# Kernel tuning notes

Measured on AMD Instinct MI355X. Metric: run time of the kernel, lower is better.

Reference implementation:

```python
import jax, jax.numpy as jnp
import numpy as np

B, S, D_MODEL, D_K = 4, 2048, 1024, 1
D_QKV = D_MODEL * D_K  # per-stream feature dim (q, k, v each)
MASK_NEG = -9000000000000000.0


def setup_inputs() -> dict:
    key = jax.random.key(0)
    kx, kw = jax.random.split(key)
    x = jax.random.normal(kx, (B, S, D_MODEL), dtype=jnp.float32)
    # Dense kernel, flax convention: [in_features, out_features], no bias
    W = jax.random.normal(kw, (D_MODEL, 3 * D_QKV), dtype=jnp.float32) * (1.0 / np.sqrt(D_MODEL))
    return {"x": x, "W": W}


def _scaled_dot_product_attention(q, k, v):
    # q,k,v: [B, S, d]
    d_k = k.shape[-1]
    scores = jnp.einsum("bqd,bkd->bqk", q, k) / jnp.sqrt(jnp.float32(d_k))
    # Faithful to source: keep upper triangle (incl. diagonal), then mask zeros.
    scores = jnp.triu(scores, k=0)
    scores = jnp.where(scores == 0, MASK_NEG, scores)
    attn = jax.nn.softmax(scores, axis=-1)
    return jnp.einsum("bqk,bkd->bqd", attn, v)


def reference(x, W) -> jnp.ndarray:
    qkv = jnp.einsum("bsd,df->bsf", x, W)  # fused QKV projection
    q, k, v = jnp.split(qkv, 3, axis=-1)
    return _scaled_dot_product_attention(q, k, v)
```

## Files before the change

### kernel.cpp

```cpp
#include <hip/hip_runtime.h>

#define SB 2048
#define DM 1024
#define N3 3072

typedef short bf16x8 __attribute__((ext_vector_type(8)));
typedef float f32x4 __attribute__((ext_vector_type(4)));
typedef unsigned short u16;

#define MFMA16(a, b, c) __builtin_amdgcn_mfma_f32_16x16x32_bf16(a, b, c, 0, 0, 0)

typedef const __attribute__((address_space(1))) unsigned int* gptr_t;
typedef __attribute__((address_space(3))) unsigned int* lptr_t;

__device__ __forceinline__ u16 f2bf(float x) {
  union { float f; unsigned u; } c; c.f = x;
  unsigned r = c.u + 0x7FFFu + ((c.u >> 16) & 1u);
  return (u16)(r >> 16);
}
__device__ __forceinline__ float bf2f(u16 x) {
  union { unsigned u; float f; } c; c.u = ((unsigned)x) << 16;
  return c.f;
}

__global__ void k_cvt_x(const float* __restrict__ x, u16* __restrict__ xb, int n4) {
  int i = blockIdx.x * blockDim.x + threadIdx.x;
  if (i >= n4) return;
  float4 v = ((const float4*)x)[i];
  ushort4 o;
  o.x = f2bf(v.x); o.y = f2bf(v.y); o.z = f2bf(v.z); o.w = f2bf(v.w);
  ((ushort4*)xb)[i] = o;
}

__global__ void k_cvt_wt(const float* __restrict__ W, u16* __restrict__ Wt) {
  __shared__ float t[32][33];
  int n0 = blockIdx.x * 32;
  int k0 = blockIdx.y * 32;
  int tx = threadIdx.x & 31, ty = threadIdx.x >> 5;
#pragma unroll
  for (int r = 0; r < 4; ++r)
    t[ty + r * 8][tx] = W[(size_t)(k0 + ty + r * 8) * N3 + n0 + tx];
  __syncthreads();
#pragma unroll
  for (int r = 0; r < 4; ++r)
    Wt[(size_t)(n0 + ty + r * 8) * DM + k0 + tx] = f2bf(t[tx][ty + r * 8]);
}

__global__ __launch_bounds__(256, 2) void k_gemm(const u16* __restrict__ xb,
                                                 const u16* __restrict__ wt,
                                                 u16* __restrict__ qk,
                                                 u16* __restrict__ vt) {
  __shared__ u16 As[2][128 * 32];
  __shared__ u16 Bs[2][128 * 32];
  int mt = blockIdx.x / 24, nt = blockIdx.x % 24;
  int m0 = mt * 128, n0 = nt * 128;
  int tid = threadIdx.x, lane = tid & 63, wid = tid >> 6;
  int lr = lane & 15, lg = lane >> 4;
  int wm = (wid >> 1) * 64, wn = (wid & 1) * 64;
  int ca = lane >> 2;
  int cb = (lane & 3) * 8;
  f32x4 acc[4][4] = {};
  int p = 0;
  for (int kk = 0; kk < 1024; kk += 32) {
#pragma unroll
    for (int j = 0; j < 2; ++j) {
      int chunk = wid * 2 + j;
      const u16* ga = xb + (size_t)(m0 + chunk * 16 + ca) * 1024 + kk + cb;
      const u16* gb = wt + (size_t)(n0 + chunk * 16 + ca) * 1024 + kk + cb;
      __builtin_amdgcn_global_load_lds((gptr_t)(const void*)ga, (lptr_t)(void*)&As[p][chunk * 512], 16, 0, 0);
      __builtin_amdgcn_global_load_lds((gptr_t)(const void*)gb, (lptr_t)(void*)&Bs[p][chunk * 512], 16, 0, 0);
    }
    __syncthreads();
    bf16x8 af[4], bff[4];
#pragma unroll
    for (int i = 0; i < 4; ++i) af[i] = *(const bf16x8*)&As[p][(wm + i * 16 + lr) * 32 + lg * 8];
#pragma unroll
    for (int j = 0; j < 4; ++j) bff[j] = *(const bf16x8*)&Bs[p][(wn + j * 16 + lr) * 32 + lg * 8];
#pragma unroll
    for (int i = 0; i < 4; ++i)
#pragma unroll
      for (int j = 0; j < 4; ++j)
        acc[i][j] = MFMA16(af[i], bff[j], acc[i][j]);
    __syncthreads();
    p ^= 1;
  }
  if (nt < 16) {
#pragma unroll
    for (int i = 0; i < 4; ++i)
#pragma unroll
      for (int j = 0; j < 4; ++j)
#pragma unroll
        for (int r = 0; r < 4; ++r)
          qk[(size_t)(m0 + wm + i * 16 + lg * 4 + r) * 2048 + n0 + wn + j * 16 + lr] = f2bf(acc[i][j][r]);
  } else {
    int d0 = n0 - 2048;
#pragma unroll
    for (int i = 0; i < 4; ++i)
#pragma unroll
      for (int j = 0; j < 4; ++j)
#pragma unroll
        for (int r = 0; r < 4; ++r) {
          int m = m0 + wm + i * 16 + lg * 4 + r;
          int d = d0 + wn + j * 16 + lr;
          vt[(size_t)((m >> 11) * DM + d) * SB + (m & 2047)] = f2bf(acc[i][j][r]);
        }
  }
}

__global__ __launch_bounds__(256, 2) void k_qkt(const u16* __restrict__ qk,
                                                u16* __restrict__ S) {
  __shared__ u16 As[2][128 * 32];
  __shared__ u16 Bs[2][128 * 32];
  int bid = blockIdx.x;
  int b = bid & 3;
  int pi = bid >> 2;
  int qt = 0;
  while (true) { int cnt = 16 - qt; if (pi < cnt) break; pi -= cnt; ++qt; }
  int kt = qt + pi;
  int m0 = qt * 128, n0 = kt * 128;
  int tid = threadIdx.x, lane = tid & 63, wid = tid >> 6;
  int lr = lane & 15, lg = lane >> 4;
  int wm = (wid >> 1) * 64, wn = (wid & 1) * 64;
  int ca = lane >> 2;
  int cb = (lane & 3) * 8;
  const u16* Qb = qk + (size_t)(b * SB) * 2048;
  f32x4 acc[4][4] = {};
  int p = 0;
  for (int kk = 0; kk < 1024; kk += 32) {
#pragma unroll
    for (int j = 0; j < 2; ++j) {
      int chunk = wid * 2 + j;
      const u16* ga = Qb + (size_t)(m0 + chunk * 16 + ca) * 2048 + kk + cb;
      const u16* gb = Qb + (size_t)(n0 + chunk * 16 + ca) * 2048 + 1024 + kk + cb;
      __builtin_amdgcn_global_load_lds((gptr_t)(const void*)ga, (lptr_t)(void*)&As[p][chunk * 512], 16, 0, 0);
      __builtin_amdgcn_global_load_lds((gptr_t)(const void*)gb, (lptr_t)(void*)&Bs[p][chunk * 512], 16, 0, 0);
    }
    __syncthreads();
    bf16x8 af[4], bff[4];
#pragma unroll
    for (int i = 0; i < 4; ++i) af[i] = *(const bf16x8*)&As[p][(wm + i * 16 + lr) * 32 + lg * 8];
#pragma unroll
    for (int j = 0; j < 4; ++j) bff[j] = *(const bf16x8*)&Bs[p][(wn + j * 16 + lr) * 32 + lg * 8];
#pragma unroll
    for (int i = 0; i < 4; ++i)
#pragma unroll
      for (int j = 0; j < 4; ++j)
        acc[i][j] = MFMA16(af[i], bff[j], acc[i][j]);
    __syncthreads();
    p ^= 1;
  }
  u16* Sb = S + (size_t)(b * SB) * 2048;
#pragma unroll
  for (int i = 0; i < 4; ++i)
#pragma unroll
    for (int j = 0; j < 4; ++j)
#pragma unroll
      for (int r = 0; r < 4; ++r) {
        int q = m0 + wm + i * 16 + lg * 4 + r;
        int k = n0 + wn + j * 16 + lr;
        float v = acc[i][j][r] * 0.03125f;
        if (k < q) v = -1e30f;
        Sb[(size_t)q * 2048 + k] = f2bf(v);
      }
}

__global__ void k_sm(u16* __restrict__ S) {
  __shared__ float rmax[4], rsum[4];
  int row = blockIdx.x;
  int q = row & 2047;
  int k0 = (q >> 7) << 7;
  int len = 2048 - k0;
  int tid = threadIdx.x;
  u16* rp = S + (size_t)row * 2048 + k0;
  int nv = len >> 3;
  bool act = tid < nv;
  float v[8];
  float mx = -1e30f;
  if (act) {
    bf16x8 x = *(const bf16x8*)(rp + tid * 8);
#pragma unroll
    for (int j = 0; j < 8; ++j) { v[j] = bf2f((u16)x[j]); mx = fmaxf(mx, v[j]); }
  }
#pragma unroll
  for (int off = 32; off; off >>= 1) mx = fmaxf(mx, __shfl_xor(mx, off, 64));
  int wv = tid >> 6;
  if ((tid & 63) == 0) rmax[wv] = mx;
  __syncthreads();
  mx = fmaxf(fmaxf(rmax[0], rmax[1]), fmaxf(rmax[2], rmax[3]));
  float sum = 0.f;
  if (act) {
#pragma unroll
    for (int j = 0; j < 8; ++j) { v[j] = __expf(v[j] - mx); sum += v[j]; }
  }
#pragma unroll
  for (int off = 32; off; off >>= 1) sum += __shfl_xor(sum, off, 64);
  if ((tid & 63) == 0) rsum[wv] = sum;
  __syncthreads();
  float inv = 1.f / ((rsum[0] + rsum[1]) + (rsum[2] + rsum[3]));
  if (act) {
    bf16x8 o;
#pragma unroll
    for (int j = 0; j < 8; ++j) o[j] = (short)f2bf(v[j] * inv);
    *(bf16x8*)(rp + tid * 8) = o;
  }
}

__global__ __launch_bounds__(256, 2) void k_pv(const u16* __restrict__ P,
                                               const u16* __restrict__ vt,
                                               float* __restrict__ out) {
  __shared__ u16 As[2][128 * 32];
  __shared__ u16 Bs[2][128 * 32];
  int bid = blockIdx.x;
  int qt = bid >> 5;
  int rem = bid & 31;
  int dt = rem >> 2;
  int b = rem & 3;
  int m0 = qt * 128, n0 = dt * 128;
  int tid = threadIdx.x, lane = tid & 63, wid = tid >> 6;
  int lr = lane & 15, lg = lane >> 4;
  int wm = (wid >> 1) * 64, wn = (wid & 1) * 64;
  int ca = lane >> 2;
  int cb = (lane & 3) * 8;
  const u16* Pb = P + (size_t)(b * SB) * 2048;
  const u16* Vb = vt + (size_t)(b * DM) * 2048;
  f32x4 acc[4][4] = {};
  int p = 0;
  for (int kk = m0; kk < 2048; kk += 32) {
#pragma unroll
    for (int j = 0; j < 2; ++j) {
      int chunk = wid * 2 + j;
      const u16* ga = Pb + (size_t)(m0 + chunk * 16 + ca) * 2048 + kk + cb;
      const u16* gb = Vb + (size_t)(n0 + chunk * 16 + ca) * 2048 + kk + cb;
      __builtin_amdgcn_global_load_lds((gptr_t)(const void*)ga, (lptr_t)(void*)&As[p][chunk * 512], 16, 0, 0);
      __builtin_amdgcn_global_load_lds((gptr_t)(const void*)gb, (lptr_t)(void*)&Bs[p][chunk * 512], 16, 0, 0);
    }
    __syncthreads();
    bf16x8 af[4], bff[4];
#pragma unroll
    for (int i = 0; i < 4; ++i) af[i] = *(const bf16x8*)&As[p][(wm + i * 16 + lr) * 32 + lg * 8];
#pragma unroll
    for (int j = 0; j < 4; ++j) bff[j] = *(const bf16x8*)&Bs[p][(wn + j * 16 + lr) * 32 + lg * 8];
#pragma unroll
    for (int i = 0; i < 4; ++i)
#pragma unroll
      for (int j = 0; j < 4; ++j)
        acc[i][j] = MFMA16(af[i], bff[j], acc[i][j]);
    __syncthreads();
    p ^= 1;
  }
#pragma unroll
  for (int i = 0; i < 4; ++i)
#pragma unroll
    for (int j = 0; j < 4; ++j)
#pragma unroll
      for (int r = 0; r < 4; ++r)
        out[(size_t)(b * SB + m0 + wm + i * 16 + lg * 4 + r) * DM + n0 + wn + j * 16 + lr] = acc[i][j][r];
}

extern "C" void kernel_launch(void* const* d_in, const int* in_sizes, int n_in,
                              void* d_out, int out_size, void* d_ws, size_t ws_size,
                              hipStream_t stream) {
  const float* x = (const float*)d_in[0];
  const float* W = (const float*)d_in[1];
  float* out = (float*)d_out;
  char* ws = (char*)d_ws;
  u16* qk = (u16*)(ws);
  u16* vt = (u16*)(ws + 33554432);
  u16* xb = (u16*)(ws + 50331648);
  u16* wt = (u16*)(ws + 67108864);
  u16* S  = (u16*)(ws + 50331648);

  k_cvt_x<<<8192, 256, 0, stream>>>(x, xb, 2097152);
  dim3 gw(96, 32);
  k_cvt_wt<<<gw, 256, 0, stream>>>(W, wt);
  k_gemm<<<1536, 256, 0, stream>>>(xb, wt, qk, vt);
  k_qkt<<<544, 256, 0, stream>>>(qk, S);
  k_sm<<<8192, 256, 0, stream>>>(S);
  k_pv<<<512, 256, 0, stream>>>(S, vt, out);
}
```

Baseline: 167.6 us.

## Restructure QKV GEMM with 128x256 tiles, 4-stage LDS pipeline and swizzle

The projection GEMM now uses 512-thread blocks computing 128x256 tiles with a four-deep global-to-LDS prefetch ring. Manual vmcnt waits and a single barrier per k-step replace the previous double-buffered load/sync/compute loop. LDS rows are XOR-style rotated to avoid bank conflicts, block ids are swizzled for L2 locality, and MFMA runs at raised priority. This aims to hide global load latency and raise MFMA utilization, at the cost of more LDS per block, which may lower occupancy.

Result: slower. 179.7 us (+7.2%).

```diff
diff --git a/kernel.cpp b/kernel.cpp
--- a/kernel.cpp
+++ b/kernel.cpp
@@ -46,63 +46,94 @@
     Wt[(size_t)(n0 + ty + r * 8) * DM + k0 + tx] = f2bf(t[tx][ty + r * 8]);
 }
 
-__global__ __launch_bounds__(256, 2) void k_gemm(const u16* __restrict__ xb,
+__global__ __launch_bounds__(512, 2) void k_gemm(const u16* __restrict__ xb,
                                                  const u16* __restrict__ wt,
                                                  u16* __restrict__ qk,
                                                  u16* __restrict__ vt) {
-  __shared__ u16 As[2][128 * 32];
-  __shared__ u16 Bs[2][128 * 32];
-  int mt = blockIdx.x / 24, nt = blockIdx.x % 24;
-  int m0 = mt * 128, n0 = nt * 128;
+  __shared__ u16 Asl[4][128 * 32];
+  __shared__ u16 Bsl[4][256 * 32];
+  int bid = blockIdx.x;
+  int swz = (bid & 7) * 96 + (bid >> 3);
+  int mt = swz / 12, nt = swz % 12;
+  int m0 = mt * 128, n0 = nt * 256;
   int tid = threadIdx.x, lane = tid & 63, wid = tid >> 6;
-  int lr = lane & 15, lg = lane >> 4;
-  int wm = (wid >> 1) * 64, wn = (wid & 1) * 64;
-  int ca = lane >> 2;
-  int cb = (lane & 3) * 8;
+  int lr = lane & 15, kg = lane >> 4;
+  int wm = (wid >> 2) * 64, wn = (wid & 3) * 64;
+
+  int arow = tid >> 2, aseg = tid & 3;
+  const u16* aptr = xb + (size_t)(m0 + arow) * 1024 + ((aseg - (arow >> 1)) & 3) * 8;
+  int brow0 = tid >> 2, brow1 = 128 + (tid >> 2), bseg = tid & 3;
+  const u16* bptr0 = wt + (size_t)(n0 + brow0) * 1024 + ((bseg - (brow0 >> 1)) & 3) * 8;
+  const u16* bptr1 = wt + (size_t)(n0 + brow1) * 1024 + ((bseg - (brow1 >> 1)) & 3) * 8;
+
   f32x4 acc[4][4] = {};
-  int p = 0;
-  for (int kk = 0; kk < 1024; kk += 32) {
-#pragma unroll
-    for (int j = 0; j < 2; ++j) {
-      int chunk = wid * 2 + j;
-      const u16* ga = xb + (size_t)(m0 + chunk * 16 + ca) * 1024 + kk + cb;
-      const u16* gb = wt + (size_t)(n0 + chunk * 16 + ca) * 1024 + kk + cb;
-      __builtin_amdgcn_global_load_lds((gptr_t)(const void*)ga, (lptr_t)(void*)&As[p][chunk * 512], 16, 0, 0);
-      __builtin_amdgcn_global_load_lds((gptr_t)(const void*)gb, (lptr_t)(void*)&Bs[p][chunk * 512], 16, 0, 0);
-    }
-    __syncthreads();
-    bf16x8 af[4], bff[4];
-#pragma unroll
-    for (int i = 0; i < 4; ++i) af[i] = *(const bf16x8*)&As[p][(wm + i * 16 + lr) * 32 + lg * 8];
-#pragma unroll
-    for (int j = 0; j < 4; ++j) bff[j] = *(const bf16x8*)&Bs[p][(wn + j * 16 + lr) * 32 + lg * 8];
-#pragma unroll
-    for (int i = 0; i < 4; ++i)
-#pragma unroll
-      for (int j = 0; j < 4; ++j)
-        acc[i][j] = MFMA16(af[i], bff[j], acc[i][j]);
-    __syncthreads();
-    p ^= 1;
-  }
-  if (nt < 16) {
-#pragma unroll
-    for (int i = 0; i < 4; ++i)
+
+#define STAGE_A(kt) __builtin_amdgcn_global_load_lds( \
+    (gptr_t)(const void*)(aptr + (kt) * 32), (lptr_t)(void*)&Asl[(kt) & 3][tid * 8], 16, 0, 0)
+#define STAGE_B(kt) do { \
+    __builtin_amdgcn_global_load_lds((gptr_t)(const void*)(bptr0 + (kt) * 32), \
+        (lptr_t)(void*)&Bsl[(kt) & 3][tid * 8], 16, 0, 0); \
+    __builtin_amdgcn_global_load_lds((gptr_t)(const void*)(bptr1 + (kt) * 32), \
+        (lptr_t)(void*)&Bsl[(kt) & 3][4096 + tid * 8], 16, 0, 0); } while (0)
+
+  STAGE_A(0); STAGE_B(0);
+  STAGE_A(1); STAGE_B(1);
+  STAGE_A(2); STAGE_B(2);
+  asm volatile("s_waitcnt vmcnt(6)" ::: "memory");
+  __builtin_amdgcn_s_barrier();
+
+  for (int i = 0; i < 32; ++i) {
+    int buf = i & 3;
+    if (i <= 28) STAGE_A(i + 3);
+    bf16x8 bfr[4], afr[4];
+#pragma unroll
+    for (int j = 0; j < 4; ++j) {
+      int row = wn + j * 16 + lr;
+      int slot = (kg + (row >> 1)) & 3;
+      bfr[j] = *(const bf16x8*)&Bsl[buf][row * 32 + slot * 8];
+    }
+#pragma unroll
+    for (int q = 0; q < 4; ++q) {
+      int row = wm + q * 16 + lr;
+      int slot = (kg + (row >> 1)) & 3;
+      afr[q] = *(const bf16x8*)&Asl[buf][row * 32 + slot * 8];
+    }
+    if (i <= 28) STAGE_B(i + 3);
+    __builtin_amdgcn_s_setprio(1);
+#pragma unroll
+    for (int q = 0; q < 4; ++q)
+#pragma unroll
+      for (int j = 0; j < 4; ++j)
+        acc[q][j] = MFMA16(afr[q], bfr[j], acc[q][j]);
+    __builtin_amdgcn_s_setprio(0);
+    if (i < 31) {
+      if (i <= 28)      asm volatile("s_waitcnt vmcnt(6)" ::: "memory");
+      else if (i == 29) asm volatile("s_waitcnt vmcnt(3)" ::: "memory");
+      else              asm volatile("s_waitcnt vmcnt(0)" ::: "memory");
+      __builtin_amdgcn_s_barrier();
+    }
+  }
+#undef STAGE_A
+#undef STAGE_B
+
+  if (n0 < 2048) {
+#pragma unroll
+    for (int q = 0; q < 4; ++q)
 #pragma unroll
       for (int j = 0; j < 4; ++j)
 #pragma unroll
         for (int r = 0; r < 4; ++r)
-          qk[(size_t)(m0 + wm + i * 16 + lg * 4 + r) * 2048 + n0 + wn + j * 16 + lr] = f2bf(acc[i][j][r]);
+          qk[(size_t)(m0 + wm + q * 16 + kg * 4 + r) * 2048 + n0 + wn + j * 16 + lr] = f2bf(acc[q][j][r]);
   } else {
-    int d0 = n0 - 2048;
-#pragma unroll
-    for (int i = 0; i < 4; ++i)
+#pragma unroll
+    for (int q = 0; q < 4; ++q)
 #pragma unroll
       for (int j = 0; j < 4; ++j)
 #pragma unroll
         for (int r = 0; r < 4; ++r) {
-          int m = m0 + wm + i * 16 + lg * 4 + r;
-          int d = d0 + wn + j * 16 + lr;
-          vt[(size_t)((m >> 11) * DM + d) * SB + (m & 2047)] = f2bf(acc[i][j][r]);
+          int m = m0 + wm + q * 16 + kg * 4 + r;
+          int d = n0 + wn + j * 16 + lr - 2048;
+          vt[(size_t)((m >> 11) * DM + d) * SB + (m & 2047)] = f2bf(acc[q][j][r]);
         }
   }
 }
@@ -273,7 +304,7 @@
   k_cvt_x<<<8192, 256, 0, stream>>>(x, xb, 2097152);
   dim3 gw(96, 32);
   k_cvt_wt<<<gw, 256, 0, stream>>>(W, wt);
-  k_gemm<<<1536, 256, 0, stream>>>(xb, wt, qk, vt);
+  k_gemm<<<768, 512, 0, stream>>>(xb, wt, qk, vt);
   k_qkt<<<544, 256, 0, stream>>>(qk, S);
   k_sm<<<8192, 256, 0, stream>>>(S);
   k_pv<<<512, 256, 0, stream>>>(S, vt, out);
```

## Add 4-buffer prefetch pipeline with swizzled LDS layout to the three GEMM kernels

Applied to the files above, without the earlier changes.

Reworks the GEMM, QK^T and PV kernels to use four LDS stages, prefetching two K-tiles ahead with global_load_lds. The previous loop synchronized twice per iteration with no overlap; the new loop uses a single s_waitcnt vmcnt plus a barrier per step. It also XOR-style rotates 16-byte segments per row pair to cut LDS bank conflicts on fragment reads, and raises wave priority around the MFMA block. LDS per block doubles to 64KB, which may limit occupancy to two blocks per CU as the launch bounds request.

Result: slower. 186.5 us (+11.3%).

```diff
diff --git a/kernel.cpp b/kernel.cpp
--- a/kernel.cpp
+++ b/kernel.cpp
@@ -21,6 +21,9 @@
 __device__ __forceinline__ float bf2f(u16 x) {
   union { unsigned u; float f; } c; c.u = ((unsigned)x) << 16;
   return c.f;
+}
+__device__ __forceinline__ void glds(const u16* g, u16* l) {
+  __builtin_amdgcn_global_load_lds((gptr_t)(const void*)g, (lptr_t)(void*)l, 16, 0, 0);
 }
 
 __global__ void k_cvt_x(const float* __restrict__ x, u16* __restrict__ xb, int n4) {
@@ -46,62 +49,82 @@
     Wt[(size_t)(n0 + ty + r * 8) * DM + k0 + tx] = f2bf(t[tx][ty + r * 8]);
 }
 
+
 __global__ __launch_bounds__(256, 2) void k_gemm(const u16* __restrict__ xb,
                                                  const u16* __restrict__ wt,
                                                  u16* __restrict__ qk,
                                                  u16* __restrict__ vt) {
-  __shared__ u16 As[2][128 * 32];
-  __shared__ u16 Bs[2][128 * 32];
-  int mt = blockIdx.x / 24, nt = blockIdx.x % 24;
+  __shared__ u16 As[4][128 * 32];
+  __shared__ u16 Bs[4][128 * 32];
+  int bid = blockIdx.x;
+  int mt = bid / 24, nt = bid % 24;
   int m0 = mt * 128, n0 = nt * 128;
   int tid = threadIdx.x, lane = tid & 63, wid = tid >> 6;
-  int lr = lane & 15, lg = lane >> 4;
+  int lr = lane & 15, kg = lane >> 4;
   int wm = (wid >> 1) * 64, wn = (wid & 1) * 64;
-  int ca = lane >> 2;
-  int cb = (lane & 3) * 8;
+  int r2 = tid >> 2, seg = tid & 3;
+  int scol = ((seg - (r2 >> 1)) & 3) * 8;
+  const u16* a0 = xb + (size_t)(m0 + r2) * 1024 + scol;
+  const u16* a1 = xb + (size_t)(m0 + 64 + r2) * 1024 + scol;
+  const u16* b0 = wt + (size_t)(n0 + r2) * 1024 + scol;
+  const u16* b1 = wt + (size_t)(n0 + 64 + r2) * 1024 + scol;
+
+#define STAGE(kt) do { int _b = (kt) & 3; int _o = (kt) * 32;            \
+    glds(a0 + _o, &As[_b][tid * 8]);                                     \
+    glds(a1 + _o, &As[_b][2048 + tid * 8]);                              \
+    glds(b0 + _o, &Bs[_b][tid * 8]);                                     \
+    glds(b1 + _o, &Bs[_b][2048 + tid * 8]); } while (0)
+
   f32x4 acc[4][4] = {};
-  int p = 0;
-  for (int kk = 0; kk < 1024; kk += 32) {
-#pragma unroll
-    for (int j = 0; j < 2; ++j) {
-      int chunk = wid * 2 + j;
-      const u16* ga = xb + (size_t)(m0 + chunk * 16 + ca) * 1024 + kk + cb;
-      const u16* gb = wt + (size_t)(n0 + chunk * 16 + ca) * 1024 + kk + cb;
-      __builtin_amdgcn_global_load_lds((gptr_t)(const void*)ga, (lptr_t)(void*)&As[p][chunk * 512], 16, 0, 0);
-      __builtin_amdgcn_global_load_lds((gptr_t)(const void*)gb, (lptr_t)(void*)&Bs[p][chunk * 512], 16, 0, 0);
-    }
-    __syncthreads();
+  STAGE(0); STAGE(1);
+  asm volatile("s_waitcnt vmcnt(4)" ::: "memory");
+  __builtin_amdgcn_s_barrier();
+  for (int t = 0; t < 32; ++t) {
+    if (t < 30) STAGE(t + 2);
+    int buf = t & 3;
     bf16x8 af[4], bff[4];
 #pragma unroll
-    for (int i = 0; i < 4; ++i) af[i] = *(const bf16x8*)&As[p][(wm + i * 16 + lr) * 32 + lg * 8];
-#pragma unroll
-    for (int j = 0; j < 4; ++j) bff[j] = *(const bf16x8*)&Bs[p][(wn + j * 16 + lr) * 32 + lg * 8];
+    for (int i = 0; i < 4; ++i) {
+      int row = wm + i * 16 + lr;
+      af[i] = *(const bf16x8*)&As[buf][row * 32 + ((kg + (row >> 1)) & 3) * 8];
+    }
+#pragma unroll
+    for (int j = 0; j < 4; ++j) {
+      int row = wn + j * 16 + lr;
+      bff[j] = *(const bf16x8*)&Bs[buf][row * 32 + ((kg + (row >> 1)) & 3) * 8];
+    }
+    __builtin_amdgcn_s_setprio(1);
 #pragma unroll
     for (int i = 0; i < 4; ++i)
 #pragma unroll
       for (int j = 0; j < 4; ++j)
         acc[i][j] = MFMA16(af[i], bff[j], acc[i][j]);
-    __syncthreads();
-    p ^= 1;
-  }
-  if (nt < 16) {
+    __builtin_amdgcn_s_setprio(0);
+    if (t < 31) {
+      if (t < 30) asm volatile("s_waitcnt vmcnt(4)" ::: "memory");
+      else        asm volatile("s_waitcnt vmcnt(0)" ::: "memory");
+      __builtin_amdgcn_s_barrier();
+    }
+  }
+#undef STAGE
+
+  if (n0 < 2048) {
 #pragma unroll
     for (int i = 0; i < 4; ++i)
 #pragma unroll
       for (int j = 0; j < 4; ++j)
 #pragma unroll
         for (int r = 0; r < 4; ++r)
-          qk[(size_t)(m0 + wm + i * 16 + lg * 4 + r) * 2048 + n0 + wn + j * 16 + lr] = f2bf(acc[i][j][r]);
+          qk[(size_t)(m0 + wm + i * 16 + kg * 4 + r) * 2048 + n0 + wn + j * 16 + lr] = f2bf(acc[i][j][r]);
   } else {
-    int d0 = n0 - 2048;
 #pragma unroll
     for (int i = 0; i < 4; ++i)
 #pragma unroll
       for (int j = 0; j < 4; ++j)
 #pragma unroll
         for (int r = 0; r < 4; ++r) {
-          int m = m0 + wm + i * 16 + lg * 4 + r;
-          int d = d0 + wn + j * 16 + lr;
+          int m = m0 + wm + i * 16 + kg * 4 + r;
+          int d = n0 + wn + j * 16 + lr - 2048;
           vt[(size_t)((m >> 11) * DM + d) * SB + (m & 2047)] = f2bf(acc[i][j][r]);
         }
   }
@@ -109,8 +132,8 @@
 
 __global__ __launch_bounds__(256, 2) void k_qkt(const u16* __restrict__ qk,
                                                 u16* __restrict__ S) {
-  __shared__ u16 As[2][128 * 32];
-  __shared__ u16 Bs[2][128 * 32];
+  __shared__ u16 As[4][128 * 32];
+  __shared__ u16 Bs[4][128 * 32];
   int bid = blockIdx.x;
   int b = bid & 3;
   int pi = bid >> 2;
@@ -119,36 +142,55 @@
   int kt = qt + pi;
   int m0 = qt * 128, n0 = kt * 128;
   int tid = threadIdx.x, lane = tid & 63, wid = tid >> 6;
-  int lr = lane & 15, lg = lane >> 4;
+  int lr = lane & 15, kg = lane >> 4;
   int wm = (wid >> 1) * 64, wn = (wid & 1) * 64;
-  int ca = lane >> 2;
-  int cb = (lane & 3) * 8;
+  int r2 = tid >> 2, seg = tid & 3;
+  int scol = ((seg - (r2 >> 1)) & 3) * 8;
   const u16* Qb = qk + (size_t)(b * SB) * 2048;
+  const u16* a0 = Qb + (size_t)(m0 + r2) * 2048 + scol;
+  const u16* a1 = Qb + (size_t)(m0 + 64 + r2) * 2048 + scol;
+  const u16* b0 = Qb + (size_t)(n0 + r2) * 2048 + 1024 + scol;
+  const u16* b1 = Qb + (size_t)(n0 + 64 + r2) * 2048 + 1024 + scol;
+
+#define STAGE(kt_) do { int _b = (kt_) & 3; int _o = (kt_) * 32;         \
+    glds(a0 + _o, &As[_b][tid * 8]);                                     \
+    glds(a1 + _o, &As[_b][2048 + tid * 8]);                              \
+    glds(b0 + _o, &Bs[_b][tid * 8]);                                     \
+    glds(b1 + _o, &Bs[_b][2048 + tid * 8]); } while (0)
+
   f32x4 acc[4][4] = {};
-  int p = 0;
-  for (int kk = 0; kk < 1024; kk += 32) {
-#pragma unroll
-    for (int j = 0; j < 2; ++j) {
-      int chunk = wid * 2 + j;
-      const u16* ga = Qb + (size_t)(m0 + chunk * 16 + ca) * 2048 + kk + cb;
-      const u16* gb = Qb + (size_t)(n0 + chunk * 16 + ca) * 2048 + 1024 + kk + cb;
-      __builtin_amdgcn_global_load_lds((gptr_t)(const void*)ga, (lptr_t)(void*)&As[p][chunk * 512], 16, 0, 0);
-      __builtin_amdgcn_global_load_lds((gptr_t)(const void*)gb, (lptr_t)(void*)&Bs[p][chunk * 512], 16, 0, 0);
-    }
-    __syncthreads();
+  STAGE(0); STAGE(1);
+  asm volatile("s_waitcnt vmcnt(4)" ::: "memory");
+  __builtin_amdgcn_s_barrier();
+  for (int t = 0; t < 32; ++t) {
+    if (t < 30) STAGE(t + 2);
+    int buf = t & 3;
     bf16x8 af[4], bff[4];
 #pragma unroll
-    for (int i = 0; i < 4; ++i) af[i] = *(const bf16x8*)&As[p][(wm + i * 16 + lr) * 32 + lg * 8];
-#pragma unroll
-    for (int j = 0; j < 4; ++j) bff[j] = *(const bf16x8*)&Bs[p][(wn + j * 16 + lr) * 32 + lg * 8];
+    for (int i = 0; i < 4; ++i) {
+      int row = wm + i * 16 + lr;
+      af[i] = *(const bf16x8*)&As[buf][row * 32 + ((kg + (row >> 1)) & 3) * 8];
+    }
+#pragma unroll
+    for (int j = 0; j < 4; ++j) {
+      int row = wn + j * 16 + lr;
+      bff[j] = *(const bf16x8*)&Bs[buf][row * 32 + ((kg + (row >> 1)) & 3) * 8];
+    }
+    __builtin_amdgcn_s_setprio(1);
 #pragma unroll
     for (int i = 0; i < 4; ++i)
 #pragma unroll
       for (int j = 0; j < 4; ++j)
         acc[i][j] = MFMA16(af[i], bff[j], acc[i][j]);
-    __syncthreads();
-    p ^= 1;
-  }
+    __builtin_amdgcn_s_setprio(0);
+    if (t < 31) {
+      if (t < 30) asm volatile("s_waitcnt vmcnt(4)" ::: "memory");
+      else        asm volatile("s_waitcnt vmcnt(0)" ::: "memory");
+      __builtin_amdgcn_s_barrier();
+    }
+  }
+#undef STAGE
+
   u16* Sb = S + (size_t)(b * SB) * 2048;
 #pragma unroll
   for (int i = 0; i < 4; ++i)
@@ -156,7 +198,7 @@
     for (int j = 0; j < 4; ++j)
 #pragma unroll
       for (int r = 0; r < 4; ++r) {
-        int q = m0 + wm + i * 16 + lg * 4 + r;
+        int q = m0 + wm + i * 16 + kg * 4 + r;
         int k = n0 + wn + j * 16 + lr;
         float v = acc[i][j][r] * 0.03125f;
         if (k < q) v = -1e30f;
@@ -208,53 +250,73 @@
 __global__ __launch_bounds__(256, 2) void k_pv(const u16* __restrict__ P,
                                                const u16* __restrict__ vt,
                                                float* __restrict__ out) {
-  __shared__ u16 As[2][128 * 32];
-  __shared__ u16 Bs[2][128 * 32];
+  __shared__ u16 As[4][128 * 32];
+  __shared__ u16 Bs[4][128 * 32];
   int bid = blockIdx.x;
   int qt = bid >> 5;
   int rem = bid & 31;
   int dt = rem >> 2;
   int b = rem & 3;
   int m0 = qt * 128, n0 = dt * 128;
+  int nkt = (2048 - m0) >> 5;
   int tid = threadIdx.x, lane = tid & 63, wid = tid >> 6;
-  int lr = lane & 15, lg = lane >> 4;
+  int lr = lane & 15, kg = lane >> 4;
   int wm = (wid >> 1) * 64, wn = (wid & 1) * 64;
-  int ca = lane >> 2;
-  int cb = (lane & 3) * 8;
+  int r2 = tid >> 2, seg = tid & 3;
+  int scol = ((seg - (r2 >> 1)) & 3) * 8;
   const u16* Pb = P + (size_t)(b * SB) * 2048;
   const u16* Vb = vt + (size_t)(b * DM) * 2048;
+  const u16* a0 = Pb + (size_t)(m0 + r2) * 2048 + m0 + scol;
+  const u16* a1 = Pb + (size_t)(m0 + 64 + r2) * 2048 + m0 + scol;
+  const u16* b0 = Vb + (size_t)(n0 + r2) * 2048 + m0 + scol;
+  const u16* b1 = Vb + (size_t)(n0 + 64 + r2) * 2048 + m0 + scol;
+
+#define STAGE(kt_) do { int _b = (kt_) & 3; int _o = (kt_) * 32;         \
+    glds(a0 + _o, &As[_b][tid * 8]);                                     \
+    glds(a1 + _o, &As[_b][2048 + tid * 8]);                              \
+    glds(b0 + _o, &Bs[_b][tid * 8]);                                     \
+    glds(b1 + _o, &Bs[_b][2048 + tid * 8]); } while (0)
+
   f32x4 acc[4][4] = {};
-  int p = 0;
-  for (int kk = m0; kk < 2048; kk += 32) {
-#pragma unroll
-    for (int j = 0; j < 2; ++j) {
-      int chunk = wid * 2 + j;
-      const u16* ga = Pb + (size_t)(m0 + chunk * 16 + ca) * 2048 + kk + cb;
-      const u16* gb = Vb + (size_t)(n0 + chunk * 16 + ca) * 2048 + kk + cb;
-      __builtin_amdgcn_global_load_lds((gptr_t)(const void*)ga, (lptr_t)(void*)&As[p][chunk * 512], 16, 0, 0);
-      __builtin_amdgcn_global_load_lds((gptr_t)(const void*)gb, (lptr_t)(void*)&Bs[p][chunk * 512], 16, 0, 0);
-    }
-    __syncthreads();
+  STAGE(0); STAGE(1);
+  asm volatile("s_waitcnt vmcnt(4)" ::: "memory");
+  __builtin_amdgcn_s_barrier();
+  for (int t = 0; t < nkt; ++t) {
+    if (t + 2 < nkt) STAGE(t + 2);
+    int buf = t & 3;
     bf16x8 af[4], bff[4];
 #pragma unroll
-    for (int i = 0; i < 4; ++i) af[i] = *(const bf16x8*)&As[p][(wm + i * 16 + lr) * 32 + lg * 8];
-#pragma unroll
-    for (int j = 0; j < 4; ++j) bff[j] = *(const bf16x8*)&Bs[p][(wn + j * 16 + lr) * 32 + lg * 8];
+    for (int i = 0; i < 4; ++i) {
+      int row = wm + i * 16 + lr;
+      af[i] = *(const bf16x8*)&As[buf][row * 32 + ((kg + (row >> 1)) & 3) * 8];
+    }
+#pragma unroll
+    for (int j = 0; j < 4; ++j) {
+      int row = wn + j * 16 + lr;
+      bff[j] = *(const bf16x8*)&Bs[buf][row * 32 + ((kg + (row >> 1)) & 3) * 8];
+    }
+    __builtin_amdgcn_s_setprio(1);
 #pragma unroll
     for (int i = 0; i < 4; ++i)
 #pragma unroll
       for (int j = 0; j < 4; ++j)
         acc[i][j] = MFMA16(af[i], bff[j], acc[i][j]);
-    __syncthreads();
-    p ^= 1;
-  }
+    __builtin_amdgcn_s_setprio(0);
+    if (t + 1 < nkt) {
+      if (t + 2 < nkt) asm volatile("s_waitcnt vmcnt(4)" ::: "memory");
+      else             asm volatile("s_waitcnt vmcnt(0)" ::: "memory");
+      __builtin_amdgcn_s_barrier();
+    }
+  }
+#undef STAGE
+
 #pragma unroll
   for (int i = 0; i < 4; ++i)
 #pragma unroll
     for (int j = 0; j < 4; ++j)
 #pragma unroll
       for (int r = 0; r < 4; ++r)
-        out[(size_t)(b * SB + m0 + wm + i * 16 + lg * 4 + r) * DM + n0 + wn + j * 16 + lr] = acc[i][j][r];
+        out[(size_t)(b * SB + m0 + wm + i * 16 + kg * 4 + r) * DM + n0 + wn + j * 16 + lr] = acc[i][j][r];
 }
 
 extern "C" void kernel_launch(void* const* d_in, const int* in_sizes, int n_in,
```

## Rewrite QKV projection GEMM with 256x256 tiles and 4-stage async pipeline

Applied to the files above, without the earlier changes.

The QKV projection GEMM now uses 256x256 tiles with 512 threads and a 4-buffer LDS ring fed by global_load_lds, prefetching two k-steps ahead. Work is split into half-steps with explicit waitcnt and barriers, plus s_setprio around the MFMA bursts. LDS columns are XOR-swizzled to avoid bank conflicts, and the block index is remapped to improve L2 locality. The aim is to hide global-load latency and raise MFMA utilization, at the cost of fewer blocks (384), one block per CU and fragile hand-written wait counts.

Result: slower. 171.9 us (+2.6%).

```diff
diff --git a/kernel.cpp b/kernel.cpp
--- a/kernel.cpp
+++ b/kernel.cpp
@@ -21,6 +21,9 @@
 __device__ __forceinline__ float bf2f(u16 x) {
   union { unsigned u; float f; } c; c.u = ((unsigned)x) << 16;
   return c.f;
+}
+__device__ __forceinline__ void glds(const u16* g, u16* l) {
+  __builtin_amdgcn_global_load_lds((gptr_t)(const void*)g, (lptr_t)(void*)l, 16, 0, 0);
 }
 
 __global__ void k_cvt_x(const float* __restrict__ x, u16* __restrict__ xb, int n4) {
@@ -46,62 +49,104 @@
     Wt[(size_t)(n0 + ty + r * 8) * DM + k0 + tx] = f2bf(t[tx][ty + r * 8]);
 }
 
-__global__ __launch_bounds__(256, 2) void k_gemm(const u16* __restrict__ xb,
+__global__ __launch_bounds__(512, 1) void k_gemm(const u16* __restrict__ xb,
                                                  const u16* __restrict__ wt,
                                                  u16* __restrict__ qk,
                                                  u16* __restrict__ vt) {
-  __shared__ u16 As[2][128 * 32];
-  __shared__ u16 Bs[2][128 * 32];
-  int mt = blockIdx.x / 24, nt = blockIdx.x % 24;
-  int m0 = mt * 128, n0 = nt * 128;
+  __shared__ u16 As[4][256 * 32];
+  __shared__ u16 Bs[4][256 * 32];
+  int bid = blockIdx.x;
+  int swz = (bid & 7) * 48 + (bid >> 3);
+  int mt = swz / 12, nt = swz % 12;
+  int m0 = mt * 256, n0 = nt * 256;
   int tid = threadIdx.x, lane = tid & 63, wid = tid >> 6;
-  int lr = lane & 15, lg = lane >> 4;
-  int wm = (wid >> 1) * 64, wn = (wid & 1) * 64;
-  int ca = lane >> 2;
-  int cb = (lane & 3) * 8;
-  f32x4 acc[4][4] = {};
-  int p = 0;
-  for (int kk = 0; kk < 1024; kk += 32) {
-#pragma unroll
-    for (int j = 0; j < 2; ++j) {
-      int chunk = wid * 2 + j;
-      const u16* ga = xb + (size_t)(m0 + chunk * 16 + ca) * 1024 + kk + cb;
-      const u16* gb = wt + (size_t)(n0 + chunk * 16 + ca) * 1024 + kk + cb;
-      __builtin_amdgcn_global_load_lds((gptr_t)(const void*)ga, (lptr_t)(void*)&As[p][chunk * 512], 16, 0, 0);
-      __builtin_amdgcn_global_load_lds((gptr_t)(const void*)gb, (lptr_t)(void*)&Bs[p][chunk * 512], 16, 0, 0);
-    }
-    __syncthreads();
-    bf16x8 af[4], bff[4];
-#pragma unroll
-    for (int i = 0; i < 4; ++i) af[i] = *(const bf16x8*)&As[p][(wm + i * 16 + lr) * 32 + lg * 8];
-#pragma unroll
-    for (int j = 0; j < 4; ++j) bff[j] = *(const bf16x8*)&Bs[p][(wn + j * 16 + lr) * 32 + lg * 8];
+  int lr = lane & 15, kg = lane >> 4;
+  int wm = (wid >> 2) * 128, wn = (wid & 3) * 64;
+  int r2 = tid >> 2, seg = tid & 3;
+  int scol = ((seg - (r2 >> 1)) & 3) * 8;
+  const u16* a0 = xb + (size_t)(m0 + r2) * 1024 + scol;
+  const u16* a1 = xb + (size_t)(m0 + 128 + r2) * 1024 + scol;
+  const u16* b0 = wt + (size_t)(n0 + r2) * 1024 + scol;
+  const u16* b1 = wt + (size_t)(n0 + 128 + r2) * 1024 + scol;
+
+#define STAGE_A(kt) do { int _b = (kt) & 3; int _o = (kt) * 32;          \
+    glds(a0 + _o, &As[_b][tid * 8]);                                     \
+    glds(a1 + _o, &As[_b][4096 + tid * 8]); } while (0)
+#define STAGE_B(kt) do { int _b = (kt) & 3; int _o = (kt) * 32;          \
+    glds(b0 + _o, &Bs[_b][tid * 8]);                                     \
+    glds(b1 + _o, &Bs[_b][4096 + tid * 8]); } while (0)
+
+  f32x4 acc[8][4] = {};
+  STAGE_A(0); STAGE_B(0);
+  STAGE_A(1); STAGE_B(1);
+  asm volatile("s_waitcnt vmcnt(4)" ::: "memory");
+  __builtin_amdgcn_s_barrier();
+
+  for (int t = 0; t < 32; ++t) {
+    int buf = t & 3;
+    bf16x8 bff[4], af[4];
+#pragma unroll
+    for (int j = 0; j < 4; ++j) {
+      int row = wn + j * 16 + lr;
+      bff[j] = *(const bf16x8*)&Bs[buf][row * 32 + ((kg + (row >> 1)) & 3) * 8];
+    }
+#pragma unroll
+    for (int i = 0; i < 4; ++i) {
+      int row = wm + i * 16 + lr;
+      af[i] = *(const bf16x8*)&As[buf][row * 32 + ((kg + (row >> 1)) & 3) * 8];
+    }
+    if (t <= 29) STAGE_A(t + 2);
+    __builtin_amdgcn_s_barrier();
+    asm volatile("s_waitcnt lgkmcnt(0)" ::: "memory");
+    __builtin_amdgcn_sched_barrier(0);
+    __builtin_amdgcn_s_setprio(1);
 #pragma unroll
     for (int i = 0; i < 4; ++i)
 #pragma unroll
       for (int j = 0; j < 4; ++j)
         acc[i][j] = MFMA16(af[i], bff[j], acc[i][j]);
-    __syncthreads();
-    p ^= 1;
-  }
-  if (nt < 16) {
+    __builtin_amdgcn_s_setprio(0);
+    __builtin_amdgcn_s_barrier();
+#pragma unroll
+    for (int i = 0; i < 4; ++i) {
+      int row = wm + 64 + i * 16 + lr;
+      af[i] = *(const bf16x8*)&As[buf][row * 32 + ((kg + (row >> 1)) & 3) * 8];
+    }
+    if (t <= 29) STAGE_B(t + 2);
+    __builtin_amdgcn_s_barrier();
+    asm volatile("s_waitcnt lgkmcnt(0)" ::: "memory");
+    __builtin_amdgcn_sched_barrier(0);
+    __builtin_amdgcn_s_setprio(1);
 #pragma unroll
     for (int i = 0; i < 4; ++i)
 #pragma unroll
       for (int j = 0; j < 4; ++j)
+        acc[4 + i][j] = MFMA16(af[i], bff[j], acc[4 + i][j]);
+    __builtin_amdgcn_s_setprio(0);
+    if (t <= 29)      asm volatile("s_waitcnt vmcnt(4)" ::: "memory");
+    else if (t == 30) asm volatile("s_waitcnt vmcnt(0)" ::: "memory");
+    __builtin_amdgcn_s_barrier();
+  }
+#undef STAGE_A
+#undef STAGE_B
+
+  if (n0 < 2048) {
+#pragma unroll
+    for (int i = 0; i < 8; ++i)
+#pragma unroll
+      for (int j = 0; j < 4; ++j)
 #pragma unroll
         for (int r = 0; r < 4; ++r)
-          qk[(size_t)(m0 + wm + i * 16 + lg * 4 + r) * 2048 + n0 + wn + j * 16 + lr] = f2bf(acc[i][j][r]);
+          qk[(size_t)(m0 + wm + i * 16 + kg * 4 + r) * 2048 + n0 + wn + j * 16 + lr] = f2bf(acc[i][j][r]);
   } else {
-    int d0 = n0 - 2048;
-#pragma unroll
-    for (int i = 0; i < 4; ++i)
+#pragma unroll
+    for (int i = 0; i < 8; ++i)
 #pragma unroll
       for (int j = 0; j < 4; ++j)
 #pragma unroll
         for (int r = 0; r < 4; ++r) {
-          int m = m0 + wm + i * 16 + lg * 4 + r;
-          int d = d0 + wn + j * 16 + lr;
+          int m = m0 + wm + i * 16 + kg * 4 + r;
+          int d = n0 + wn + j * 16 + lr - 2048;
           vt[(size_t)((m >> 11) * DM + d) * SB + (m & 2047)] = f2bf(acc[i][j][r]);
         }
   }
@@ -132,8 +177,8 @@
       int chunk = wid * 2 + j;
       const u16* ga = Qb + (size_t)(m0 + chunk * 16 + ca) * 2048 + kk + cb;
       const u16* gb = Qb + (size_t)(n0 + chunk * 16 + ca) * 2048 + 1024 + kk + cb;
-      __builtin_amdgcn_global_load_lds((gptr_t)(const void*)ga, (lptr_t)(void*)&As[p][chunk * 512], 16, 0, 0);
-      __builtin_amdgcn_global_load_lds((gptr_t)(const void*)gb, (lptr_t)(void*)&Bs[p][chunk * 512], 16, 0, 0);
+      glds(ga, &As[p][chunk * 512]);
+      glds(gb, &Bs[p][chunk * 512]);
     }
     __syncthreads();
     bf16x8 af[4], bff[4];
@@ -231,8 +276,8 @@
       int chunk = wid * 2 + j;
       const u16* ga = Pb + (size_t)(m0 + chunk * 16 + ca) * 2048 + kk + cb;
       const u16* gb = Vb + (size_t)(n0 + chunk * 16 + ca) * 2048 + kk + cb;
-      __builtin_amdgcn_global_load_lds((gptr_t)(const void*)ga, (lptr_t)(void*)&As[p][chunk * 512], 16, 0, 0);
-      __builtin_amdgcn_global_load_lds((gptr_t)(const void*)gb, (lptr_t)(void*)&Bs[p][chunk * 512], 16, 0, 0);
+      glds(ga, &As[p][chunk * 512]);
+      glds(gb, &Bs[p][chunk * 512]);
     }
     __syncthreads();
     bf16x8 af[4], bff[4];
@@ -273,7 +318,7 @@
   k_cvt_x<<<8192, 256, 0, stream>>>(x, xb, 2097152);
   dim3 gw(96, 32);
   k_cvt_wt<<<gw, 256, 0, stream>>>(W, wt);
-  k_gemm<<<1536, 256, 0, stream>>>(xb, wt, qk, vt);
+  k_gemm<<<384, 512, 0, stream>>>(xb, wt, qk, vt);
   k_qkt<<<544, 256, 0, stream>>>(qk, S);
   k_sm<<<8192, 256, 0, stream>>>(S);
   k_pv<<<512, 256, 0, stream>>>(S, vt, out);
```
